# Kernel tuning notes

Hardware: AMD Instinct MI355X
Metric: run time of the kernel (lower is better)

The kernel has to match this reference:

```python
import jax, jax.numpy as jnp
import numpy as np

B, L, D = 8, 2048, 1024

def setup_inputs() -> dict:
    key = jax.random.key(0)
    ks = jax.random.split(key, 4)
    s = 1.0 / np.sqrt(D)  # linear init scale
    x = jax.random.normal(ks[0], (B, L, D), dtype=jnp.float32)
    mask = jnp.zeros((B, L, L), dtype=jnp.float32)  # additive attention mask
    Wq = jax.random.normal(ks[1], (D, D), dtype=jnp.float32) * s
    Wk = jax.random.normal(ks[2], (D, D), dtype=jnp.float32) * s
    Wv = jax.random.normal(ks[3], (D, D), dtype=jnp.float32) * s
    bq = jnp.zeros((D,), dtype=jnp.float32)
    bk = jnp.zeros((D,), dtype=jnp.float32)
    bv = jnp.zeros((D,), dtype=jnp.float32)
    return {"x": x, "mask": mask, "Wq": Wq, "bq": bq, "Wk": Wk, "bk": bk, "Wv": Wv, "bv": bv}

def reference(x, mask, Wq, bq, Wk, bk, Wv, bv):
    # Linear projections (torch Linear: y = x @ W.T + b)
    q = jnp.einsum('bld,ed->ble', x, Wq) + bq
    k = jnp.einsum('bld,ed->ble', x, Wk) + bk
    v = jnp.einsum('bld,ed->ble', x, Wv) + bv
    d = x.shape[2]
    logits = jnp.einsum('bqd,bkd->bqk', q, k) / jnp.sqrt(jnp.float32(d))
    probas = jax.nn.softmax(logits + mask, axis=2)
    return jnp.einsum('bqk,bkd->bqd', probas, v)
```

## Files before the change

kernel.cpp:

```cpp
#include <hip/hip_runtime.h>
#include <hip/hip_bf16.h>

typedef __attribute__((ext_vector_type(8))) short short8;
typedef __attribute__((ext_vector_type(4))) float floatx4;

__device__ __forceinline__ unsigned short f2bf(float f) {
    unsigned int u = __builtin_bit_cast(unsigned int, f);
    u += 0x7fffu + ((u >> 16) & 1u);
    return (unsigned short)(u >> 16);
}

__device__ __forceinline__ void gl_lds16(const unsigned short* g, unsigned short* l) {
    __builtin_amdgcn_global_load_lds(
        (const __attribute__((address_space(1))) unsigned int*)(const void*)g,
        (__attribute__((address_space(3))) unsigned int*)(void*)l,
        16, 0, 0);
}

#define BM 256
#define BN 256
#define BK 64

template<bool OUT_BF16>
__global__ __launch_bounds__(512, 2)
void gemm_bt(const unsigned short* __restrict__ A,
             const unsigned short* __restrict__ B,
             void* __restrict__ O, const float* __restrict__ bias,
             int bias_mode, int K, int lda, int ldb, int ldo,
             long long aBS, long long bBS, long long oBS,
             float scale, int nby)
{
    __shared__ __align__(16) unsigned short lds[2][2][BM * BK];

    const int t = threadIdx.x;
    const int lane = t & 63;
    const int w = t >> 6;
    const int wr = w >> 2;
    const int wc = w & 3;
    const int lq = lane >> 4;
    const int lr = lane & 15;

    const int nwg = gridDim.x;
    const int swz = (blockIdx.x & 7) * (nwg >> 3) + (blockIdx.x >> 3);
    const int by = swz % nby, bx = swz / nby;
    const size_t m0 = (size_t)bx * BM, n0 = (size_t)by * BN;

    const int z = blockIdx.z;
    const unsigned short* Az = A + (size_t)z * aBS;
    const unsigned short* Bz = B + (size_t)z * bBS;

    const int srow = t >> 3;
    const int scol = ((t & 7) ^ (srow & 7)) << 3;

    floatx4 acc[8][4];
#pragma unroll
    for (int i = 0; i < 8; ++i)
#pragma unroll
        for (int j = 0; j < 4; ++j)
            acc[i][j] = (floatx4){0.f, 0.f, 0.f, 0.f};

    const int NT = K / BK;

    auto stage = [&](int mat, int u, int kt, int buf) {
        const unsigned short* g = (mat ? Bz + (n0 + u * 64 + srow) * (size_t)ldb
                                       : Az + (m0 + u * 64 + srow) * (size_t)lda) + kt + scol;
        gl_lds16(g, &lds[buf][mat][u * 4096 + w * 512]);
    };

#pragma unroll
    for (int u = 0; u < 4; ++u) stage(1, u, 0, 0);
#pragma unroll
    for (int u = 0; u < 4; ++u) stage(0, u, 0, 0);
    if (NT > 1) {
#pragma unroll
        for (int u = 0; u < 4; ++u) stage(1, u, BK, 1);
        asm volatile("s_waitcnt vmcnt(4)" ::: "memory");
    } else {
        asm volatile("s_waitcnt vmcnt(0)" ::: "memory");
    }
    __builtin_amdgcn_s_barrier();
    __builtin_amdgcn_sched_barrier(0);

    for (int tt = 0; tt < NT; ++tt) {
        const int cur = tt & 1, nxt = cur ^ 1;
        const int kt1 = (tt + 1) * BK, kt2 = (tt + 2) * BK;
        short8 bfr[4][2];
#pragma unroll
        for (int p = 0; p < 4; ++p) {
            short8 af[2][2];
            if (p == 0) {
#pragma unroll
                for (int ni = 0; ni < 4; ++ni)
#pragma unroll
                    for (int kk = 0; kk < 2; ++kk) {
                        const int rb = wc * 64 + ni * 16 + lr;
                        const int j = kk * 4 + lq;
                        bfr[ni][kk] = *(const short8*)&lds[cur][1][rb * 64 + ((j ^ (rb & 7)) << 3)];
                    }
            }
#pragma unroll
            for (int mi2 = 0; mi2 < 2; ++mi2)
#pragma unroll
                for (int kk = 0; kk < 2; ++kk) {
                    const int ra = wr * 128 + (2 * p + mi2) * 16 + lr;
                    const int j = kk * 4 + lq;
                    af[mi2][kk] = *(const short8*)&lds[cur][0][ra * 64 + ((j ^ (ra & 7)) << 3)];
                }
            if (p == 0 && tt + 1 < NT) { stage(0, 0, kt1, nxt); stage(0, 1, kt1, nxt); }
            if (p == 1 && tt + 1 < NT) { stage(0, 2, kt1, nxt); stage(0, 3, kt1, nxt); }
            if (p == 2 && tt + 2 < NT) { stage(1, 0, kt2, cur); stage(1, 1, kt2, cur); }
            if (p == 3 && tt + 2 < NT) { stage(1, 2, kt2, cur); stage(1, 3, kt2, cur); }

            __builtin_amdgcn_sched_barrier(0);
            __builtin_amdgcn_s_barrier();
            __builtin_amdgcn_sched_barrier(0);
            __builtin_amdgcn_s_setprio(1);
#pragma unroll
            for (int kk = 0; kk < 2; ++kk)
#pragma unroll
                for (int mi2 = 0; mi2 < 2; ++mi2)
#pragma unroll
                    for (int ni = 0; ni < 4; ++ni)
                        acc[2 * p + mi2][ni] = __builtin_amdgcn_mfma_f32_16x16x32_bf16(
                            af[mi2][kk], bfr[ni][kk], acc[2 * p + mi2][ni], 0, 0, 0);
            __builtin_amdgcn_s_setprio(0);
            __builtin_amdgcn_sched_barrier(0);
            if (p == 3) {
                if (tt < NT - 2) asm volatile("s_waitcnt vmcnt(4)" ::: "memory");
                else             asm volatile("s_waitcnt vmcnt(0)" ::: "memory");
            }
            __builtin_amdgcn_s_barrier();
            __builtin_amdgcn_sched_barrier(0);
        }
    }

#pragma unroll
    for (int mi = 0; mi < 8; ++mi) {
#pragma unroll
        for (int ni = 0; ni < 4; ++ni) {
            const size_t col = n0 + wc * 64 + ni * 16 + lr;
            const float cb = (bias_mode == 1) ? bias[col] : 0.f;
            floatx4 v = acc[mi][ni];
#pragma unroll
            for (int r = 0; r < 4; ++r) {
                const size_t row = m0 + wr * 128 + mi * 16 + lq * 4 + r;
                float val = v[r] * scale + cb;
                if (bias_mode == 2) val += bias[row];
                if (OUT_BF16)
                    ((unsigned short*)O)[(size_t)z * oBS + row * (size_t)ldo + col] = f2bf(val);
                else
                    ((float*)O)[(size_t)z * oBS + row * (size_t)ldo + col] = val;
            }
        }
    }
}

__global__ void cvt_f2b(const float4* __restrict__ src, ushort4* __restrict__ dst, int n4)
{
    int i = blockIdx.x * blockDim.x + threadIdx.x;
    const int stride = gridDim.x * blockDim.x;
    for (; i < n4; i += stride) {
        float4 f = src[i];
        dst[i] = (ushort4){f2bf(f.x), f2bf(f.y), f2bf(f.z), f2bf(f.w)};
    }
}

__global__ void softmax_kernel(float* __restrict__ S, const float* __restrict__ mask, int b0)
{
    const int lane = threadIdx.x & 63;
    const int wid = threadIdx.x >> 6;
    const size_t rowid = (size_t)blockIdx.x * 4 + wid;
    const size_t bi = rowid >> 11;
    const size_t q = rowid & 2047;
    float* Srow = S + rowid * 2048;
    const float* Mrow = mask + (((size_t)b0 + bi) * 2048 + q) * 2048;

    float4 v[8];
    float mx = -3.4e38f;
#pragma unroll
    for (int i = 0; i < 8; ++i) {
        float4 s = ((const float4*)Srow)[i * 64 + lane];
        float4 m = ((const float4*)Mrow)[i * 64 + lane];
        s.x += m.x; s.y += m.y; s.z += m.z; s.w += m.w;
        v[i] = s;
        mx = fmaxf(mx, fmaxf(fmaxf(s.x, s.y), fmaxf(s.z, s.w)));
    }
#pragma unroll
    for (int off = 32; off; off >>= 1) mx = fmaxf(mx, __shfl_xor(mx, off, 64));
    float sum = 0.f;
#pragma unroll
    for (int i = 0; i < 8; ++i) {
        v[i].x = __expf(v[i].x - mx);
        v[i].y = __expf(v[i].y - mx);
        v[i].z = __expf(v[i].z - mx);
        v[i].w = __expf(v[i].w - mx);
        sum += v[i].x + v[i].y + v[i].z + v[i].w;
    }
#pragma unroll
    for (int off = 32; off; off >>= 1) sum += __shfl_xor(sum, off, 64);
    const float inv = 1.0f / sum;

    unsigned short* Prow = (unsigned short*)Srow;
#pragma unroll
    for (int i = 0; i < 8; ++i) {
        ushort4 h = {f2bf(v[i].x * inv), f2bf(v[i].y * inv),
                     f2bf(v[i].z * inv), f2bf(v[i].w * inv)};
        ((ushort4*)Prow)[i * 64 + lane] = h;
    }
}

extern "C" void kernel_launch(void* const* d_in, const int* in_sizes, int n_in,
                              void* d_out, int out_size, void* d_ws, size_t ws_size,
                              hipStream_t stream)
{
    const float* x    = (const float*)d_in[0];
    const float* mask = (const float*)d_in[1];
    const float* Wq   = (const float*)d_in[2];
    const float* bq   = (const float*)d_in[3];
    const float* Wk   = (const float*)d_in[4];
    const float* bk   = (const float*)d_in[5];
    const float* Wv   = (const float*)d_in[6];
    const float* bv   = (const float*)d_in[7];
    float* out = (float*)d_out;

    const size_t MB = 1ull << 20;
    char* ws = (char*)d_ws;
    unsigned short* Qb  = (unsigned short*)(ws);
    unsigned short* Kb  = (unsigned short*)(ws + 32 * MB);
    unsigned short* Vt  = (unsigned short*)(ws + 64 * MB);
    unsigned short* Wqb = (unsigned short*)(ws + 96 * MB);
    unsigned short* Wkb = (unsigned short*)(ws + 98 * MB);
    unsigned short* Wvb = (unsigned short*)(ws + 100 * MB);
    unsigned short* xb  = (unsigned short*)(ws + 102 * MB);
    float* Sb = (float*)(ws + 102 * MB);

    size_t savail = (ws_size > 102 * MB) ? ws_size - 102 * MB : 0;
    int g = 1;
    if (savail >= 128 * MB) g = 8;
    else if (savail >= 64 * MB) g = 4;
    else if (savail >= 32 * MB) g = 2;

    dim3 blk(512, 1, 1);

    cvt_f2b<<<2048, 256, 0, stream>>>((const float4*)x, (ushort4*)xb, 16384 * 1024 / 4);
    cvt_f2b<<<512, 256, 0, stream>>>((const float4*)Wq, (ushort4*)Wqb, 1024 * 1024 / 4);
    cvt_f2b<<<512, 256, 0, stream>>>((const float4*)Wk, (ushort4*)Wkb, 1024 * 1024 / 4);
    cvt_f2b<<<512, 256, 0, stream>>>((const float4*)Wv, (ushort4*)Wvb, 1024 * 1024 / 4);

    gemm_bt<true><<<dim3(256, 1, 1), blk, 0, stream>>>(
        xb, Wqb, Qb, bq, 1, 1024, 1024, 1024, 1024, 0LL, 0LL, 0LL, 1.0f, 4);
    gemm_bt<true><<<dim3(256, 1, 1), blk, 0, stream>>>(
        xb, Wkb, Kb, bk, 1, 1024, 1024, 1024, 1024, 0LL, 0LL, 0LL, 1.0f, 4);
    gemm_bt<true><<<dim3(256, 1, 1), blk, 0, stream>>>(
        Wvb, xb, Vt, bv, 2, 1024, 1024, 1024, 16384, 0LL, 0LL, 0LL, 1.0f, 64);

    const float sscale = 0.03125f;
    for (int b0 = 0; b0 < 8; b0 += g) {
        const int gb = (8 - b0 < g) ? (8 - b0) : g;
        gemm_bt<false><<<dim3(64, 1, gb), blk, 0, stream>>>(
            Qb + (size_t)b0 * 2048 * 1024, Kb + (size_t)b0 * 2048 * 1024, Sb,
            (const float*)nullptr, 0, 1024, 1024, 1024, 2048,
            2048LL * 1024, 2048LL * 1024, 2048LL * 2048, sscale, 8);
        softmax_kernel<<<dim3(gb * 512, 1, 1), dim3(256), 0, stream>>>(Sb, mask, b0);
        gemm_bt<false><<<dim3(32, 1, gb), blk, 0, stream>>>(
            (const unsigned short*)Sb, Vt + (size_t)b0 * 2048,
            out + (size_t)b0 * 2048 * 1024, (const float*)nullptr, 0,
            2048, 4096, 16384, 1024,
            2048LL * 4096, 2048LL, 2048LL * 1024, 1.0f, 4);
    }
}
```

Before: 557.0 us.

## Fuse QKV projections into one GEMM and store attention scores in fp16

Merges the four fp32-to-bf16 conversion launches into one kernel. Concatenates Wq/Wk/Wv so a single 768-block GEMM produces interleaved Q|K plus a transposed V, written through an LDS-swizzled epilogue. Logits are stored as fp16 rather than fp32, which halves score traffic for the QK GEMM and the softmax and allows more batches per chunk. The aim is fewer launches, less memory traffic and better GPU fill, at the cost of fp16 range and precision on the logits and extra epilogue complexity.

```diff
diff --git a/kernel.cpp b/kernel.cpp
--- a/kernel.cpp
+++ b/kernel.cpp
@@ -1,7 +1,10 @@
 #include <hip/hip_runtime.h>
 #include <hip/hip_bf16.h>
+#include <hip/hip_fp16.h>
 
 typedef __attribute__((ext_vector_type(8))) short short8;
+typedef __attribute__((ext_vector_type(4))) short sh4;
+typedef __attribute__((ext_vector_type(8))) _Float16 half8;
 typedef __attribute__((ext_vector_type(4))) float floatx4;
 
 __device__ __forceinline__ unsigned short f2bf(float f) {
@@ -21,14 +24,17 @@
 #define BN 256
 #define BK 64
 
-template<bool OUT_BF16>
+template<int OMODE>
 __global__ __launch_bounds__(512, 2)
 void gemm_bt(const unsigned short* __restrict__ A,
              const unsigned short* __restrict__ B,
-             void* __restrict__ O, const float* __restrict__ bias,
-             int bias_mode, int K, int lda, int ldb, int ldo,
+             void* __restrict__ O,
+             const float* __restrict__ bias0, const float* __restrict__ bias1,
+             const float* __restrict__ bias2,
+             int K, int lda, int ldb, int ldo,
              long long aBS, long long bBS, long long oBS,
-             float scale, int nby)
+             float scale, int nby, int vstart,
+             unsigned short* __restrict__ Vt, int ldvt)
 {
     __shared__ __align__(16) unsigned short lds[2][2][BM * BK];
 
@@ -134,78 +140,132 @@
         }
     }
 
-#pragma unroll
-    for (int mi = 0; mi < 8; ++mi) {
-#pragma unroll
-        for (int ni = 0; ni < 4; ++ni) {
-            const size_t col = n0 + wc * 64 + ni * 16 + lr;
-            const float cb = (bias_mode == 1) ? bias[col] : 0.f;
-            floatx4 v = acc[mi][ni];
-#pragma unroll
-            for (int r = 0; r < 4; ++r) {
-                const size_t row = m0 + wr * 128 + mi * 16 + lq * 4 + r;
-                float val = v[r] * scale + cb;
-                if (bias_mode == 2) val += bias[row];
-                if (OUT_BF16)
-                    ((unsigned short*)O)[(size_t)z * oBS + row * (size_t)ldo + col] = f2bf(val);
-                else
-                    ((float*)O)[(size_t)z * oBS + row * (size_t)ldo + col] = val;
-            }
-        }
-    }
-}
-
-__global__ void cvt_f2b(const float4* __restrict__ src, ushort4* __restrict__ dst, int n4)
+    const float* bias = bias0; int cshift = 0;
+    if (bias1) {
+        const int r = (int)(n0 >> 10);
+        bias = (r == 0) ? bias0 : ((r == 1) ? bias1 : bias2);
+        cshift = r << 10;
+    }
+
+    if (vstart >= 0 && (int)n0 >= vstart) {
+        unsigned short* lf = &lds[0][0][0] + w * 8192;
+        __syncthreads();
+#pragma unroll
+        for (int mi = 0; mi < 8; ++mi) {
+#pragma unroll
+            for (int ni = 0; ni < 4; ++ni) {
+                const int tc = ni * 16 + lr;
+                const int col = (int)n0 + wc * 64 + tc;
+                const float cb = bias ? bias[col - cshift] : 0.f;
+                const int tr0 = mi * 16 + lq * 4;
+                floatx4 v = acc[mi][ni];
+                sh4 pk;
+#pragma unroll
+                for (int r = 0; r < 4; ++r) pk[r] = (short)f2bf(v[r] * scale + cb);
+                *(sh4*)&lf[tc * 128 + (tr0 ^ ((tc & 7) << 3))] = pk;
+            }
+        }
+        __syncthreads();
+        const int vrow_base = (int)n0 - vstart + wc * 64;
+        const size_t colb = m0 + (size_t)wr * 128 + (size_t)(lane & 15) * 8;
+#pragma unroll
+        for (int i = 0; i < 16; ++i) {
+            const int vr = i * 4 + (lane >> 4);
+            short8 d = *(const short8*)&lf[vr * 128 + (((lane & 15) * 8) ^ ((vr & 7) << 3))];
+            *(short8*)&Vt[(size_t)(vrow_base + vr) * ldvt + colb] = d;
+        }
+    } else {
+#pragma unroll
+        for (int mi = 0; mi < 8; ++mi) {
+#pragma unroll
+            for (int ni = 0; ni < 4; ++ni) {
+                const size_t col = n0 + wc * 64 + ni * 16 + lr;
+                const float cb = bias ? bias[col - cshift] : 0.f;
+                floatx4 v = acc[mi][ni];
+#pragma unroll
+                for (int r = 0; r < 4; ++r) {
+                    const size_t row = m0 + wr * 128 + mi * 16 + lq * 4 + r;
+                    const float val = v[r] * scale + cb;
+                    const size_t off = (size_t)z * oBS + row * (size_t)ldo + col;
+                    if (OMODE == 0)
+                        ((unsigned short*)O)[off] = f2bf(val);
+                    else if (OMODE == 1)
+                        ((float*)O)[off] = val;
+                    else {
+                        _Float16 h = (_Float16)val;
+                        ((unsigned short*)O)[off] = __builtin_bit_cast(unsigned short, h);
+                    }
+                }
+            }
+        }
+    }
+}
+
+__global__ void cvt4(const float4* __restrict__ s0, ushort4* __restrict__ d0, int n0,
+                     const float4* __restrict__ s1, ushort4* __restrict__ d1, int n1,
+                     const float4* __restrict__ s2, ushort4* __restrict__ d2, int n2,
+                     const float4* __restrict__ s3, ushort4* __restrict__ d3, int n3)
 {
-    int i = blockIdx.x * blockDim.x + threadIdx.x;
+    const int total = n0 + n1 + n2 + n3;
     const int stride = gridDim.x * blockDim.x;
-    for (; i < n4; i += stride) {
-        float4 f = src[i];
-        dst[i] = (ushort4){f2bf(f.x), f2bf(f.y), f2bf(f.z), f2bf(f.w)};
-    }
-}
-
-__global__ void softmax_kernel(float* __restrict__ S, const float* __restrict__ mask, int b0)
+    for (int i = blockIdx.x * blockDim.x + threadIdx.x; i < total; i += stride) {
+        const float4* s; ushort4* d; int j = i;
+        if (j < n0) { s = s0; d = d0; }
+        else { j -= n0;
+            if (j < n1) { s = s1; d = d1; }
+            else { j -= n1;
+                if (j < n2) { s = s2; d = d2; }
+                else { j -= n2; s = s3; d = d3; }
+            }
+        }
+        float4 f = s[j];
+        d[j] = (ushort4){f2bf(f.x), f2bf(f.y), f2bf(f.z), f2bf(f.w)};
+    }
+}
+
+__global__ void softmax_kernel(_Float16* __restrict__ S, const float* __restrict__ mask, int b0)
 {
     const int lane = threadIdx.x & 63;
     const int wid = threadIdx.x >> 6;
     const size_t rowid = (size_t)blockIdx.x * 4 + wid;
     const size_t bi = rowid >> 11;
     const size_t q = rowid & 2047;
-    float* Srow = S + rowid * 2048;
+    _Float16* Srow = S + rowid * 2048;
     const float* Mrow = mask + (((size_t)b0 + bi) * 2048 + q) * 2048;
 
-    float4 v[8];
+    float v[32];
     float mx = -3.4e38f;
 #pragma unroll
-    for (int i = 0; i < 8; ++i) {
-        float4 s = ((const float4*)Srow)[i * 64 + lane];
-        float4 m = ((const float4*)Mrow)[i * 64 + lane];
-        s.x += m.x; s.y += m.y; s.z += m.z; s.w += m.w;
-        v[i] = s;
-        mx = fmaxf(mx, fmaxf(fmaxf(s.x, s.y), fmaxf(s.z, s.w)));
+    for (int i = 0; i < 4; ++i) {
+        half8 h = ((const half8*)Srow)[i * 64 + lane];
+        float4 ma = ((const float4*)Mrow)[i * 128 + lane * 2];
+        float4 mb = ((const float4*)Mrow)[i * 128 + lane * 2 + 1];
+        const float* mp0 = (const float*)&ma;
+        const float* mp1 = (const float*)&mb;
+#pragma unroll
+        for (int j = 0; j < 4; ++j) {
+            v[i * 8 + j]     = (float)h[j]     + mp0[j];
+            v[i * 8 + 4 + j] = (float)h[4 + j] + mp1[j];
+        }
+#pragma unroll
+        for (int j = 0; j < 8; ++j) mx = fmaxf(mx, v[i * 8 + j]);
     }
 #pragma unroll
     for (int off = 32; off; off >>= 1) mx = fmaxf(mx, __shfl_xor(mx, off, 64));
     float sum = 0.f;
 #pragma unroll
-    for (int i = 0; i < 8; ++i) {
-        v[i].x = __expf(v[i].x - mx);
-        v[i].y = __expf(v[i].y - mx);
-        v[i].z = __expf(v[i].z - mx);
-        v[i].w = __expf(v[i].w - mx);
-        sum += v[i].x + v[i].y + v[i].z + v[i].w;
-    }
+    for (int i = 0; i < 32; ++i) { v[i] = __expf(v[i] - mx); sum += v[i]; }
 #pragma unroll
     for (int off = 32; off; off >>= 1) sum += __shfl_xor(sum, off, 64);
     const float inv = 1.0f / sum;
 
     unsigned short* Prow = (unsigned short*)Srow;
 #pragma unroll
-    for (int i = 0; i < 8; ++i) {
-        ushort4 h = {f2bf(v[i].x * inv), f2bf(v[i].y * inv),
-                     f2bf(v[i].z * inv), f2bf(v[i].w * inv)};
-        ((ushort4*)Prow)[i * 64 + lane] = h;
+    for (int i = 0; i < 4; ++i) {
+        short8 pk;
+#pragma unroll
+        for (int j = 0; j < 8; ++j) pk[j] = (short)f2bf(v[i * 8 + j] * inv);
+        ((short8*)Prow)[i * 64 + lane] = pk;
     }
 }
 
@@ -225,47 +285,41 @@
 
     const size_t MB = 1ull << 20;
     char* ws = (char*)d_ws;
-    unsigned short* Qb  = (unsigned short*)(ws);
-    unsigned short* Kb  = (unsigned short*)(ws + 32 * MB);
-    unsigned short* Vt  = (unsigned short*)(ws + 64 * MB);
-    unsigned short* Wqb = (unsigned short*)(ws + 96 * MB);
-    unsigned short* Wkb = (unsigned short*)(ws + 98 * MB);
-    unsigned short* Wvb = (unsigned short*)(ws + 100 * MB);
-    unsigned short* xb  = (unsigned short*)(ws + 102 * MB);
-    float* Sb = (float*)(ws + 102 * MB);
-
-    size_t savail = (ws_size > 102 * MB) ? ws_size - 102 * MB : 0;
-    int g = 1;
-    if (savail >= 128 * MB) g = 8;
-    else if (savail >= 64 * MB) g = 4;
-    else if (savail >= 32 * MB) g = 2;
-
-    dim3 blk(512, 1, 1);
-
-    cvt_f2b<<<2048, 256, 0, stream>>>((const float4*)x, (ushort4*)xb, 16384 * 1024 / 4);
-    cvt_f2b<<<512, 256, 0, stream>>>((const float4*)Wq, (ushort4*)Wqb, 1024 * 1024 / 4);
-    cvt_f2b<<<512, 256, 0, stream>>>((const float4*)Wk, (ushort4*)Wkb, 1024 * 1024 / 4);
-    cvt_f2b<<<512, 256, 0, stream>>>((const float4*)Wv, (ushort4*)Wvb, 1024 * 1024 / 4);
-
-    gemm_bt<true><<<dim3(256, 1, 1), blk, 0, stream>>>(
-        xb, Wqb, Qb, bq, 1, 1024, 1024, 1024, 1024, 0LL, 0LL, 0LL, 1.0f, 4);
-    gemm_bt<true><<<dim3(256, 1, 1), blk, 0, stream>>>(
-        xb, Wkb, Kb, bk, 1, 1024, 1024, 1024, 1024, 0LL, 0LL, 0LL, 1.0f, 4);
-    gemm_bt<true><<<dim3(256, 1, 1), blk, 0, stream>>>(
-        Wvb, xb, Vt, bv, 2, 1024, 1024, 1024, 16384, 0LL, 0LL, 0LL, 1.0f, 64);
+    unsigned short* QKb  = (unsigned short*)(ws);
+    unsigned short* Vt   = (unsigned short*)(ws + 64 * MB);
+    unsigned short* Wcat = (unsigned short*)(ws + 96 * MB);
+    unsigned short* xb   = (unsigned short*)(ws + 102 * MB);
+    _Float16* Sb         = (_Float16*)(ws + 134 * MB);
+
+    size_t savail = (ws_size > 134 * MB) ? ws_size - 134 * MB : 0;
+    int g = (int)(savail / (8 * MB));
+    if (g < 1) g = 1;
+    if (g > 8) g = 8;
+
+    cvt4<<<2048, 256, 0, stream>>>(
+        (const float4*)x,  (ushort4*)xb,               16384 * 1024 / 4,
+        (const float4*)Wq, (ushort4*)Wcat,             1024 * 1024 / 4,
+        (const float4*)Wk, (ushort4*)(Wcat + 1048576), 1024 * 1024 / 4,
+        (const float4*)Wv, (ushort4*)(Wcat + 2097152), 1024 * 1024 / 4);
+
+    gemm_bt<0><<<dim3(768, 1, 1), dim3(512), 0, stream>>>(
+        xb, Wcat, QKb, bq, bk, bv,
+        1024, 1024, 1024, 2048, 0LL, 0LL, 0LL, 1.0f, 12, 2048, Vt, 16384);
 
     const float sscale = 0.03125f;
     for (int b0 = 0; b0 < 8; b0 += g) {
         const int gb = (8 - b0 < g) ? (8 - b0) : g;
-        gemm_bt<false><<<dim3(64, 1, gb), blk, 0, stream>>>(
-            Qb + (size_t)b0 * 2048 * 1024, Kb + (size_t)b0 * 2048 * 1024, Sb,
-            (const float*)nullptr, 0, 1024, 1024, 1024, 2048,
-            2048LL * 1024, 2048LL * 1024, 2048LL * 2048, sscale, 8);
-        softmax_kernel<<<dim3(gb * 512, 1, 1), dim3(256), 0, stream>>>(Sb, mask, b0);
-        gemm_bt<false><<<dim3(32, 1, gb), blk, 0, stream>>>(
-            (const unsigned short*)Sb, Vt + (size_t)b0 * 2048,
-            out + (size_t)b0 * 2048 * 1024, (const float*)nullptr, 0,
-            2048, 4096, 16384, 1024,
-            2048LL * 4096, 2048LL, 2048LL * 1024, 1.0f, 4);
-    }
-}
+        gemm_bt<2><<<dim3(64, 1, gb), dim3(512), 0, stream>>>(
+            QKb + (size_t)b0 * 4194304, QKb + 1024 + (size_t)b0 * 4194304, Sb,
+            nullptr, nullptr, nullptr,
+            1024, 2048, 2048, 2048,
+            4194304LL, 4194304LL, 4194304LL, sscale, 8, -1, nullptr, 0);
+        softmax_kernel<<<dim3(gb * 512), dim3(256), 0, stream>>>(Sb, mask, b0);
+        gemm_bt<1><<<dim3(32, 1, gb), dim3(512), 0, stream>>>(
+            (const unsigned short*)(void*)Sb, Vt + (size_t)b0 * 2048,
+            out + (size_t)b0 * 2048 * 1024,
+            nullptr, nullptr, nullptr,
+            2048, 2048, 16384, 1024,
+            4194304LL, 2048LL, 2097152LL, 1.0f, 4, -1, nullptr, 0);
+    }
+}
```

Measured after the change: 506.0 us. -9.1%, faster.
